# Kernel tuning notes

Measured on AMD Instinct MI355X. Metric: run time of the kernel, lower is better.

The kernel has to match this reference:

```python
import jax, jax.numpy as jnp
import numpy as np

D_MODEL, D_STATE, D_CONV, EXPAND = 1024, 16, 4, 2
D_INNER = EXPAND * D_MODEL
BATCH, SEQ = 2, 2048


def setup_inputs() -> dict:
    key = jax.random.key(0)
    ks = jax.random.split(key, 10)
    s = lambda fan_in: 1.0 / np.sqrt(fan_in)
    return {
        "x": jax.random.normal(ks[0], (BATCH, SEQ, D_MODEL), jnp.float32),
        "W_in": jax.random.normal(ks[1], (2 * D_INNER, D_MODEL), jnp.float32) * s(D_MODEL),
        "w_conv": jax.random.normal(ks[2], (D_INNER, D_CONV), jnp.float32) * s(D_CONV),
        "b_conv": jax.random.normal(ks[3], (D_INNER,), jnp.float32) * 0.02,
        "W_x": jax.random.normal(ks[4], (D_INNER + 2 * D_STATE, D_INNER), jnp.float32) * s(D_INNER),
        "W_dt": jax.random.normal(ks[5], (D_INNER, D_INNER), jnp.float32) * s(D_INNER),
        "b_dt": jax.random.normal(ks[6], (D_INNER,), jnp.float32) * 0.02,
        "A_log": jnp.log(jax.random.uniform(ks[7], (D_INNER, D_STATE), jnp.float32, 1e-4, 1.0)),
        "D": jnp.ones((D_INNER,), jnp.float32),
        "W_out": jax.random.normal(ks[8], (D_MODEL, D_INNER), jnp.float32) * s(D_INNER),
    }


def _depthwise_causal_conv(x, w, b):
    # x: (B, L, C), w: (C, K), causal (left-pad K-1), matches conv1d(padding=K-1)[..., :L]
    K = w.shape[1]
    L = x.shape[1]
    xp = jnp.pad(x, ((0, 0), (K - 1, 0), (0, 0)))
    out = b
    for k in range(K):  # K is tiny (4)
        out = out + xp[:, k:k + L, :] * w[:, k]
    return out


def _selective_scan(x, delta, Bm, Cm, A, Dv):
    # x, delta: (B, L, d_inner); Bm, Cm: (B, L, d_state)
    def step(state, inp):
        x_t, d_t, B_t, C_t = inp  # (B,d_inner),(B,d_inner),(B,d_state),(B,d_state)
        decay = jnp.exp(d_t[..., None] * A)          # (B, d_inner, d_state)
        state = decay * state + B_t[:, None, :] * x_t[..., None]
        y_t = jnp.einsum('bds,bs->bd', state, C_t) + x_t * Dv
        return state, y_t

    init = jnp.zeros((x.shape[0], x.shape[2], A.shape[1]), x.dtype)
    xs = tuple(jnp.swapaxes(a, 0, 1) for a in (x, delta, Bm, Cm))
    _, ys = jax.lax.scan(step, init, xs)             # ys: (L, B, d_inner)
    return jnp.swapaxes(ys, 0, 1)


def reference(x, W_in, w_conv, b_conv, W_x, W_dt, b_dt, A_log, D, W_out):
    silu = jax.nn.silu
    xz = x @ W_in.T                                   # (B, L, 2*d_inner)
    x_inner, z = jnp.split(xz, 2, axis=-1)
    x_conv = silu(_depthwise_causal_conv(x_inner, w_conv, b_conv))
    x_dbl = x_conv @ W_x.T                            # (B, L, d_inner + 2*d_state)
    delta, Bm, Cm = jnp.split(x_dbl, [D_INNER, D_INNER + D_STATE], axis=-1)
    delta = jax.nn.softplus(delta @ W_dt.T + b_dt)
    A = -jnp.exp(A_log.astype(jnp.float32))
    y = _selective_scan(x_conv, delta, Bm, Cm, A, D)
    y = y * silu(z)
    return y @ W_out.T
```

## Files before the change

kernel.cpp:

```cpp
#include <hip/hip_runtime.h>
#include <hip/hip_bf16.h>


#define BATCH 2
#define SEQ   2048
#define DM    1024
#define DI    2048
#define DS    16
#define T_TOK (BATCH * SEQ)

#define CL 64
#define NC 32

typedef __bf16 v8bf __attribute__((ext_vector_type(8)));
typedef float  v4f  __attribute__((ext_vector_type(4)));

__device__ __forceinline__ void gld16(const void* g, void* l) {
    __builtin_amdgcn_global_load_lds(
        (const __attribute__((address_space(1))) void*)g,
        (__attribute__((address_space(3))) void*)l, 16, 0, 0);
}

__device__ __forceinline__ float b2f(__hip_bfloat16 v) { return __bfloat162float(v); }

__global__ void detect_dtype(const unsigned* __restrict__ Dptr, int* __restrict__ flag) {
    if (threadIdx.x == 0 && blockIdx.x == 0)
        *flag = (Dptr[0] == 0x3F803F80u) ? 1 : 0;
}

__device__ __forceinline__ float load_in(const void* p, size_t i, int isbf) {
    return isbf ? b2f(((const __hip_bfloat16*)p)[i]) : ((const float*)p)[i];
}

#define NBIG0 (T_TOK * DM)
#define NBIG1 (4096 * DM)
#define NBIG2 (DI * DI)
#define NBIG3 (DM * DI)
__global__ void convert_big(const void* __restrict__ s0, const void* __restrict__ s1,
                            const void* __restrict__ s2, const void* __restrict__ s3,
                            __hip_bfloat16* __restrict__ d0, __hip_bfloat16* __restrict__ d1,
                            __hip_bfloat16* __restrict__ d2, __hip_bfloat16* __restrict__ d3,
                            const int* __restrict__ flag) {
    if (*flag) return;
    size_t e = ((size_t)blockIdx.x * 256 + threadIdx.x) * 8;
    const float* src; __hip_bfloat16* dst;
    if (e < NBIG0)                      { src = (const float*)s0 + e;                 dst = d0 + e; }
    else if (e < NBIG0 + NBIG1)         { e -= NBIG0; src = (const float*)s1 + e;     dst = d1 + e; }
    else if (e < NBIG0 + NBIG1 + NBIG2) { e -= NBIG0 + NBIG1; src = (const float*)s2 + e; dst = d2 + e; }
    else                                { e -= NBIG0 + NBIG1 + NBIG2; src = (const float*)s3 + e; dst = d3 + e; }
    const float4 a = *(const float4*)src;
    const float4 b = *(const float4*)(src + 4);
    __bf16 o[8] = {(__bf16)a.x,(__bf16)a.y,(__bf16)a.z,(__bf16)a.w,
                   (__bf16)b.x,(__bf16)b.y,(__bf16)b.z,(__bf16)b.w};
    *(uint4*)dst = *(uint4*)&o[0];
}

__global__ void convert_small(const void* __restrict__ wconv, const void* __restrict__ bconv,
                              const void* __restrict__ bdt, const void* __restrict__ dv,
                              __hip_bfloat16* __restrict__ wconvb, __hip_bfloat16* __restrict__ bconvb,
                              __hip_bfloat16* __restrict__ bdtb, __hip_bfloat16* __restrict__ db,
                              const int* __restrict__ flag) {
    const int isbf = *flag;
    const int i = blockIdx.x * 256 + threadIdx.x;
    if (i < 8192)        wconvb[i]        = __float2bfloat16(load_in(wconv, i, isbf));
    else if (i < 10240)  bconvb[i - 8192] = __float2bfloat16(load_in(bconv, i - 8192, isbf));
    else if (i < 12288)  bdtb[i - 10240]  = __float2bfloat16(load_in(bdt, i - 10240, isbf));
    else if (i < 14336)  db[i - 12288]    = __float2bfloat16(load_in(dv, i - 12288, isbf));
}

template <int MODE, int KDIM>
__global__ __launch_bounds__(512, 2) void gemm8p(
    const __hip_bfloat16* __restrict__ Ac, const void* __restrict__ Araw,
    const __hip_bfloat16* __restrict__ Bc, const void* __restrict__ Braw,
    void* __restrict__ out0, void* __restrict__ out1,
    const __hip_bfloat16* __restrict__ bias,
    const int* __restrict__ flag,
    int N)
{
    constexpr int NT = KDIM >> 5;
    __shared__ v8bf lds[8192];

    const int isbf = *flag;
    const __hip_bfloat16* A  = (isbf && Araw) ? (const __hip_bfloat16*)Araw : Ac;
    const __hip_bfloat16* Bw = (isbf && Braw) ? (const __hip_bfloat16*)Braw : Bc;

    const int nx = gridDim.x;
    const int nblk = nx * gridDim.y;
    const int id = blockIdx.y * nx + blockIdx.x;
    const int sid = (id & 7) * (nblk >> 3) + (id >> 3);
    const int bm = (sid / nx) * 256;
    const int bn = (sid % nx) * 256;

    const int tid   = threadIdx.x;
    const int lane  = tid & 63;
    const int w     = tid >> 6;
    const int wr    = (w >> 2) * 128;
    const int wc    = (w & 3) * 64;
    const int lrow  = lane & 15;
    const int lquad = lane >> 4;
    const int swz   = lquad ^ ((lrow >> 1) & 3);

    v4f acc[8][4];
#pragma unroll
    for (int i = 0; i < 8; i++)
#pragma unroll
        for (int j = 0; j < 4; j++) acc[i][j] = (v4f){0.f, 0.f, 0.f, 0.f};

    const int r0 = tid >> 2;
    const int q0 = (tid & 3) ^ ((r0 >> 1) & 3);
    const __hip_bfloat16* gA0 = A  + (size_t)(bm + r0) * KDIM + q0 * 8;
    const __hip_bfloat16* gA1 = gA0 + (size_t)128 * KDIM;
    const __hip_bfloat16* gB0 = Bw + (size_t)(bn + r0) * KDIM + q0 * 8;
    const __hip_bfloat16* gB1 = gB0 + (size_t)128 * KDIM;
    char* lbase = (char*)&lds[0] + tid * 16;

    int sA[8], sB[4];
#pragma unroll
    for (int i = 0; i < 8; i++) sA[i] = (wr + i * 16 + lrow) * 4 + swz;
#pragma unroll
    for (int i = 0; i < 4; i++) sB[i] = 1024 + (wc + i * 16 + lrow) * 4 + swz;

#define STAGE8(kt, b) do {                         \
        const size_t ko_ = (size_t)(kt) * 32;      \
        char* d_ = lbase + (b) * 32768;            \
        gld16(gA0 + ko_, d_);                      \
        gld16(gA1 + ko_, d_ + 8192);               \
        gld16(gB0 + ko_, d_ + 16384);              \
        gld16(gB1 + ko_, d_ + 24576);              \
    } while (0)

    STAGE8(0, 0);
    STAGE8(1, 1);
    STAGE8(2, 2);

#pragma unroll 4
    for (int t = 0; t < NT; ++t) {
        const int cb = t & 3;
        if (t + 3 < NT) {
            STAGE8(t + 3, (t + 3) & 3);
            asm volatile("s_waitcnt vmcnt(12)" ::: "memory");
        } else if (t + 3 == NT) {
            asm volatile("s_waitcnt vmcnt(8)" ::: "memory");
        } else if (t + 2 == NT) {
            asm volatile("s_waitcnt vmcnt(4)" ::: "memory");
        } else {
            asm volatile("s_waitcnt vmcnt(0)" ::: "memory");
        }
        __builtin_amdgcn_s_barrier();

        const v8bf* buf = &lds[0] + cb * 2048;
        v8bf af[8], bfr[4];
#pragma unroll
        for (int i = 0; i < 8; i++) af[i] = buf[sA[i]];
#pragma unroll
        for (int i = 0; i < 4; i++) bfr[i] = buf[sB[i]];
        asm volatile("s_waitcnt lgkmcnt(0)" ::: "memory");
        __builtin_amdgcn_s_barrier();

        __builtin_amdgcn_s_setprio(1);
#pragma unroll
        for (int mi = 0; mi < 8; mi++)
#pragma unroll
            for (int ni = 0; ni < 4; ni++)
                acc[mi][ni] = __builtin_amdgcn_mfma_f32_16x16x32_bf16(
                    af[mi], bfr[ni], acc[mi][ni], 0, 0, 0);
        __builtin_amdgcn_s_setprio(0);
    }
#undef STAGE8

#pragma unroll
    for (int mi = 0; mi < 8; mi++) {
#pragma unroll
        for (int ni = 0; ni < 4; ni++) {
#pragma unroll
            for (int r = 0; r < 4; r++) {
                const int grow = bm + wr + mi * 16 + lquad * 4 + r;
                const int gcol = bn + wc + ni * 16 + lrow;
                const float v = acc[mi][ni][r];
                if (MODE == 0) {
                    ((__hip_bfloat16*)out0)[(size_t)grow * N + gcol] = __float2bfloat16(v);
                } else if (MODE == 1) {
                    if (gcol < 2048) {
                        ((__hip_bfloat16*)out0)[(size_t)grow * 2048 + gcol] = __float2bfloat16(v);
                    } else if (gcol < 2080) {
                        ((float*)out1)[(size_t)grow * 32 + (gcol - 2048)] = v;
                    }
                } else {
                    const float x = v + b2f(bias[gcol]);
                    const float sp = (x > 15.f) ? x : __logf(1.f + __expf(x));
                    ((__hip_bfloat16*)out0)[(size_t)grow * 2048 + gcol] = __float2bfloat16(sp);
                }
            }
        }
    }
}

template <int MODE, int TN>
__global__ __launch_bounds__(256) void gemm_bt(
    const __hip_bfloat16* __restrict__ Ac, const void* __restrict__ Araw,
    const __hip_bfloat16* __restrict__ Bc, const void* __restrict__ Braw,
    void* __restrict__ out0, void* __restrict__ out1,
    const __hip_bfloat16* __restrict__ bias,
    const int* __restrict__ flag,
    int M, int N, int K)
{
    constexpr int NF = TN / 32;
    constexpr int ASLOT = 512;
    constexpr int BSLOT = TN * 4;
    __shared__ v8bf Asv[2 * ASLOT];
    __shared__ v8bf Bsv[2 * BSLOT];

    const int isbf = *flag;
    const __hip_bfloat16* A  = (isbf && Araw) ? (const __hip_bfloat16*)Araw : Ac;
    const __hip_bfloat16* Bw = (isbf && Braw) ? (const __hip_bfloat16*)Braw : Bc;

    const int nx = gridDim.x;
    const int nblk = nx * gridDim.y;
    const int id = blockIdx.y * nx + blockIdx.x;
    const int sid = (id & 7) * (nblk >> 3) + (id >> 3);
    const int bxs = sid % nx;
    const int bys = sid / nx;

    const int tid  = threadIdx.x;
    const int bm   = bys * 128;
    const int bn   = bxs * TN;
    const int w    = tid >> 6;
    const int lane = tid & 63;
    const int wm   = (w >> 1) * 64;
    const int wn   = (w & 1) * (TN / 2);
    const int lrow  = lane & 15;
    const int lquad = lane >> 4;

    v4f acc[4][NF];
#pragma unroll
    for (int i = 0; i < 4; i++)
#pragma unroll
        for (int j = 0; j < NF; j++) acc[i][j] = (v4f){0.f, 0.f, 0.f, 0.f};

    const int r0 = tid >> 2;
    const int q0 = (tid & 3) ^ ((r0 >> 1) & 3);
    const __hip_bfloat16* gA0 = A  + (size_t)(bm + r0) * K + q0 * 8;
    const __hip_bfloat16* gA1 = A  + (size_t)(bm + 64 + r0) * K + q0 * 8;
    const __hip_bfloat16* gB0 = Bw + (size_t)(bn + r0) * K + q0 * 8;
    const __hip_bfloat16* gB1 = Bw + (size_t)(bn + 64 + r0) * K + q0 * 8;
    char* lA0 = (char*)Asv + tid * 16;
    char* lA1 = (char*)Asv + 4096 + tid * 16;
    char* lB0 = (char*)Bsv + tid * 16;
    char* lB1 = (char*)Bsv + 4096 + tid * 16;

    const int swz = lquad ^ ((lrow >> 1) & 3);
    int sA[4], sB[NF];
#pragma unroll
    for (int i = 0; i < 4; i++) sA[i] = (wm + i * 16 + lrow) * 4 + swz;
#pragma unroll
    for (int i = 0; i < NF; i++) sB[i] = (wn + i * 16 + lrow) * 4 + swz;

    const int NIT = K >> 5;
    gld16(gA0, lA0);
    gld16(gA1, lA1);
    gld16(gB0, lB0);
    if (TN == 128) gld16(gB1, lB1);

    int k = 32;
    for (int it = 0; it < NIT; ++it) {
        const int cb = it & 1;
        __syncthreads();
        if (it + 1 < NIT) {
            const int pa = (cb ^ 1) * 8192;
            const int pb = (cb ^ 1) * (BSLOT * 16);
            gld16(gA0 + k, lA0 + pa);
            gld16(gA1 + k, lA1 + pa);
            gld16(gB0 + k, lB0 + pb);
            if (TN == 128) gld16(gB1 + k, lB1 + pb);
            k += 32;
        }
        const int ca = cb * ASLOT;
        const int cbb = cb * BSLOT;
        v8bf af[4], bfr[NF];
#pragma unroll
        for (int i = 0; i < 4; i++)
            af[i] = Asv[ca + sA[i]];
#pragma unroll
        for (int i = 0; i < NF; i++)
            bfr[i] = Bsv[cbb + sB[i]];
#pragma unroll
        for (int mi = 0; mi < 4; mi++)
#pragma unroll
            for (int ni = 0; ni < NF; ni++)
                acc[mi][ni] = __builtin_amdgcn_mfma_f32_16x16x32_bf16(
                    af[mi], bfr[ni], acc[mi][ni], 0, 0, 0);
    }

#pragma unroll
    for (int mi = 0; mi < 4; mi++) {
#pragma unroll
        for (int ni = 0; ni < NF; ni++) {
#pragma unroll
            for (int r = 0; r < 4; r++) {
                const int grow = bm + wm + mi * 16 + lquad * 4 + r;
                const int gcol = bn + wn + ni * 16 + lrow;
                const float v = acc[mi][ni][r];
                if (MODE == 0) {
                    ((__hip_bfloat16*)out0)[(size_t)grow * N + gcol] = __float2bfloat16(v);
                } else if (MODE == 1) {
                    if (gcol < 2048) {
                        ((__hip_bfloat16*)out0)[(size_t)grow * 2048 + gcol] = __float2bfloat16(v);
                    } else if (gcol < 2080) {
                        ((float*)out1)[(size_t)grow * 32 + (gcol - 2048)] = v;
                    }
                } else if (MODE == 2) {
                    const float x = v + b2f(bias[gcol]);
                    const float sp = (x > 15.f) ? x : __logf(1.f + __expf(x));
                    ((__hip_bfloat16*)out0)[(size_t)grow * 2048 + gcol] = __float2bfloat16(sp);
                } else {
                    if (isbf)
                        ((__hip_bfloat16*)out0)[(size_t)grow * N + gcol] = __float2bfloat16(v);
                    else
                        ((float*)out0)[(size_t)grow * N + gcol] = v;
                }
            }
        }
    }
}

__global__ void prep_A(const void* __restrict__ A_log, float* __restrict__ Amat,
                       const int* __restrict__ flag) {
    const int isbf = *flag;
    const int i = blockIdx.x * 256 + threadIdx.x;
    if (i < DI * DS) Amat[i] = -__expf(load_in(A_log, i, isbf));
}

__global__ void pad_Wx(const void* __restrict__ Wx, __hip_bfloat16* __restrict__ Wxp,
                       const int* __restrict__ flag) {
    const int isbf = *flag;
    const size_t e = ((size_t)blockIdx.x * 256 + threadIdx.x) * 8;
    if (e >= (size_t)2304 * 2048) return;
    if (e >= (size_t)2080 * 2048) {
        __bf16 z[8] = {};
        *(uint4*)(Wxp + e) = *(uint4*)&z[0];
        return;
    }
    if (isbf) {
        *(uint4*)(Wxp + e) = *(const uint4*)((const __hip_bfloat16*)Wx + e);
    } else {
        const float* src = (const float*)Wx + e;
        const float4 a = *(const float4*)src;
        const float4 b = *(const float4*)(src + 4);
        __bf16 o[8] = {(__bf16)a.x,(__bf16)a.y,(__bf16)a.z,(__bf16)a.w,
                       (__bf16)b.x,(__bf16)b.y,(__bf16)b.z,(__bf16)b.w};
        *(uint4*)(Wxp + e) = *(uint4*)&o[0];
    }
}

__global__ __launch_bounds__(256) void conv_silu(
    const __hip_bfloat16* __restrict__ xz,
    const __hip_bfloat16* __restrict__ wconv,
    const __hip_bfloat16* __restrict__ bconv,
    __hip_bfloat16* __restrict__ xconv)
{
    const int idx = blockIdx.x * 256 + threadIdx.x;
    const int c8 = (idx & 255) << 3;
    const int tg = idx >> 8;
    const int tl = tg & (SEQ - 1);

    __bf16 wl[32], bl[8];
    *(uint4*)&wl[0]  = *(const uint4*)(wconv + c8 * 4);
    *(uint4*)&wl[8]  = *(const uint4*)(wconv + c8 * 4 + 8);
    *(uint4*)&wl[16] = *(const uint4*)(wconv + c8 * 4 + 16);
    *(uint4*)&wl[24] = *(const uint4*)(wconv + c8 * 4 + 24);
    *(uint4*)&bl[0]  = *(const uint4*)(bconv + c8);

    float acc[8];
#pragma unroll
    for (int cc = 0; cc < 8; cc++) acc[cc] = (float)bl[cc];

#pragma unroll
    for (int k = 0; k < 4; k++) {
        const int ts = tl - 3 + k;
        if (ts >= 0) {
            __bf16 xl[8];
            *(uint4*)&xl[0] = *(const uint4*)(xz + (size_t)(tg - 3 + k) * 4096 + c8);
#pragma unroll
            for (int cc = 0; cc < 8; cc++)
                acc[cc] += (float)wl[cc * 4 + k] * (float)xl[cc];
        }
    }

    __bf16 o[8];
#pragma unroll
    for (int cc = 0; cc < 8; cc++) {
        const float s = acc[cc] / (1.f + __expf(-acc[cc]));
        o[cc] = (__bf16)s;
    }
    *(uint4*)(xconv + (size_t)tg * DI + c8) = *(uint4*)&o[0];
}

__global__ __launch_bounds__(256) void scan_p1(
    const __hip_bfloat16* __restrict__ delta, const __hip_bfloat16* __restrict__ xconv,
    const float* __restrict__ BC, const float* __restrict__ Amat,
    float* __restrict__ Pws, float* __restrict__ Sws)
{
    const int d = blockIdx.x * 256 + threadIdx.x;
    const int c = blockIdx.y;
    const int b = blockIdx.z;
    const int tg0 = b * SEQ + c * CL;

    __shared__ float bc[CL * 32];
    for (int i = threadIdx.x; i < CL * 32; i += 256) bc[i] = BC[(size_t)tg0 * 32 + i];
    __syncthreads();

    float Areg[DS];
#pragma unroll
    for (int s = 0; s < DS; s++) Areg[s] = Amat[d * DS + s];

    float P[DS], S[DS];
#pragma unroll
    for (int s = 0; s < DS; s++) { P[s] = 1.f; S[s] = 0.f; }

    for (int i = 0; i < CL; i++) {
        const size_t tg = tg0 + i;
        const float dl = b2f(delta[tg * DI + d]);
        const float x  = b2f(xconv[tg * DI + d]);
#pragma unroll
        for (int s = 0; s < DS; s++) {
            const float e = __expf(dl * Areg[s]);
            P[s] *= e;
            S[s] = e * S[s] + bc[i * 32 + s] * x;
        }
    }

    const size_t base = (((size_t)b * NC + c) * DI + d) * DS;
#pragma unroll
    for (int s = 0; s < DS; s += 4) {
        *(float4*)(Pws + base + s) = make_float4(P[s], P[s+1], P[s+2], P[s+3]);
        *(float4*)(Sws + base + s) = make_float4(S[s], S[s+1], S[s+2], S[s+3]);
    }
}

__global__ void scan_p2(float* __restrict__ Pws, float* __restrict__ Sws) {
    const int idx = blockIdx.x * 256 + threadIdx.x;
    const int b  = idx >> 15;
    const int ds = idx & 32767;
    float carry = 0.f;
    for (int c = 0; c < NC; c++) {
        const size_t a = (((size_t)b * NC + c) << 15) + ds;
        const float p  = Pws[a];
        const float sv = Sws[a];
        Sws[a] = carry;
        carry = p * carry + sv;
    }
}

__global__ __launch_bounds__(256) void scan_p3(
    const __hip_bfloat16* __restrict__ delta, const __hip_bfloat16* __restrict__ xconv,
    const float* __restrict__ BC, const float* __restrict__ Amat,
    const float* __restrict__ Sws, const __hip_bfloat16* __restrict__ xz,
    const __hip_bfloat16* __restrict__ Dv, __hip_bfloat16* __restrict__ yg)
{
    const int d = blockIdx.x * 256 + threadIdx.x;
    const int c = blockIdx.y;
    const int b = blockIdx.z;
    const int tg0 = b * SEQ + c * CL;

    __shared__ float bc[CL * 32];
    for (int i = threadIdx.x; i < CL * 32; i += 256) bc[i] = BC[(size_t)tg0 * 32 + i];
    __syncthreads();

    float Areg[DS];
#pragma unroll
    for (int s = 0; s < DS; s++) Areg[s] = Amat[d * DS + s];

    const size_t base = (((size_t)b * NC + c) * DI + d) * DS;
    float S[DS];
#pragma unroll
    for (int s = 0; s < DS; s += 4) {
        const float4 v = *(const float4*)(Sws + base + s);
        S[s] = v.x; S[s+1] = v.y; S[s+2] = v.z; S[s+3] = v.w;
    }
    const float Dd = b2f(Dv[d]);

    for (int i = 0; i < CL; i++) {
        const size_t tg = tg0 + i;
        const float dl = b2f(delta[tg * DI + d]);
        const float x  = b2f(xconv[tg * DI + d]);
        float y = 0.f;
#pragma unroll
        for (int s = 0; s < DS; s++) {
            const float e = __expf(dl * Areg[s]);
            S[s] = e * S[s] + bc[i * 32 + s] * x;
            y += S[s] * bc[i * 32 + 16 + s];
        }
        y += x * Dd;
        const float z = b2f(xz[tg * 4096 + 2048 + d]);
        const float g = z / (1.f + __expf(-z));
        yg[tg * DI + d] = __float2bfloat16(y * g);
    }
}

extern "C" void kernel_launch(void* const* d_in, const int* in_sizes, int n_in,
                              void* d_out, int out_size, void* d_ws, size_t ws_size,
                              hipStream_t stream)
{
    const void* x_raw     = d_in[0];
    const void* W_in_raw  = d_in[1];
    const void* wconv_raw = d_in[2];
    const void* bconv_raw = d_in[3];
    const void* W_x_raw   = d_in[4];
    const void* W_dt_raw  = d_in[5];
    const void* b_dt_raw  = d_in[6];
    const void* A_log_raw = d_in[7];
    const void* D_raw     = d_in[8];
    const void* W_out_raw = d_in[9];

    char* ws = (char*)d_ws;
    size_t off = 0;
    auto alloc = [&](size_t bytes) { char* p = ws + off; off += (bytes + 255) & ~(size_t)255; return p; };
    int*            FLAG  = (int*)alloc(256);
    __hip_bfloat16* XB    = (__hip_bfloat16*)alloc((size_t)T_TOK * DM * 2);
    __hip_bfloat16* WINB  = (__hip_bfloat16*)alloc((size_t)4096 * DM * 2);
    __hip_bfloat16* WDTB  = (__hip_bfloat16*)alloc((size_t)DI * DI * 2);
    __hip_bfloat16* WOUTB = (__hip_bfloat16*)alloc((size_t)DM * DI * 2);
    __hip_bfloat16* WCONVB= (__hip_bfloat16*)alloc((size_t)DI * 4 * 2);
    __hip_bfloat16* BCONVB= (__hip_bfloat16*)alloc((size_t)DI * 2);
    __hip_bfloat16* BDTB  = (__hip_bfloat16*)alloc((size_t)DI * 2);
    __hip_bfloat16* DB    = (__hip_bfloat16*)alloc((size_t)DI * 2);
    __hip_bfloat16* XZ    = (__hip_bfloat16*)alloc((size_t)T_TOK * 4096 * 2);
    __hip_bfloat16* XCONV = (__hip_bfloat16*)alloc((size_t)T_TOK * DI * 2);
    __hip_bfloat16* DRAW  = (__hip_bfloat16*)alloc((size_t)T_TOK * DI * 2);
    __hip_bfloat16* WXPAD = (__hip_bfloat16*)alloc((size_t)2304 * DI * 2);
    float*          BC    = (float*)alloc((size_t)T_TOK * 32 * 4);
    __hip_bfloat16* DELTA = (__hip_bfloat16*)alloc((size_t)T_TOK * DI * 2);
    float*          AMAT  = (float*)alloc((size_t)DI * DS * 4);
    float*          PWS   = (float*)alloc((size_t)BATCH * NC * DI * DS * 4);
    float*          SWS   = (float*)alloc((size_t)BATCH * NC * DI * DS * 4);
    __hip_bfloat16* YG    = (__hip_bfloat16*)alloc((size_t)T_TOK * DI * 2);

    detect_dtype<<<1, 64, 0, stream>>>((const unsigned*)D_raw, FLAG);
    convert_big<<<(NBIG0 + NBIG1 + NBIG2 + NBIG3) / (256 * 8), 256, 0, stream>>>(
        x_raw, W_in_raw, W_dt_raw, W_out_raw, XB, WINB, WDTB, WOUTB, FLAG);
    convert_small<<<56, 256, 0, stream>>>(wconv_raw, bconv_raw, b_dt_raw, D_raw,
                                          WCONVB, BCONVB, BDTB, DB, FLAG);
    prep_A<<<(DI * DS + 255) / 256, 256, 0, stream>>>(A_log_raw, AMAT, FLAG);
    pad_Wx<<<(int)(((size_t)2304 * 2048 / 8 + 255) / 256), 256, 0, stream>>>(W_x_raw, WXPAD, FLAG);

    gemm8p<0, 1024><<<dim3(16, 16), 512, 0, stream>>>(
        XB, x_raw, WINB, W_in_raw, XZ, nullptr, nullptr, FLAG, 4096);

    conv_silu<<<T_TOK, 256, 0, stream>>>(XZ, WCONVB, BCONVB, XCONV);

    gemm8p<1, 2048><<<dim3(9, 16), 512, 0, stream>>>(
        XCONV, nullptr, WXPAD, nullptr, DRAW, BC, nullptr, FLAG, 2304);

    gemm8p<2, 2048><<<dim3(8, 16), 512, 0, stream>>>(
        DRAW, nullptr, WDTB, W_dt_raw, DELTA, nullptr, BDTB, FLAG, 2048);

    scan_p1<<<dim3(DI / 256, NC, BATCH), 256, 0, stream>>>(DELTA, XCONV, BC, AMAT, PWS, SWS);
    scan_p2<<<(BATCH * DI * DS) / 256, 256, 0, stream>>>(PWS, SWS);
    scan_p3<<<dim3(DI / 256, NC, BATCH), 256, 0, stream>>>(DELTA, XCONV, BC, AMAT, SWS, XZ, DB, YG);

    gemm_bt<3, 64><<<dim3(16, 32), 256, 0, stream>>>(
        YG, nullptr, WOUTB, W_out_raw, d_out, nullptr, nullptr, FLAG, T_TOK, DM, DI);
}
```

Baseline: 468.7 us.

## Split GEMM k-step into two half-phases interleaving LDS reads, prefetch and MFMA

Restructures the GEMM main loop into two phases per k-tile. Each phase issues half the global-to-LDS prefetch and half the A-fragment LDS reads, then runs 16 MFMAs, with barriers and the vmcnt waits rebalanced between phases. The aim is to overlap LDS reads and global loads with matrix-core work instead of loading everything before computing. It adds more barriers per iteration, and the hand-tuned vmcnt accounting must stay correct for the tail iterations.

```diff
diff --git a/kernel.cpp b/kernel.cpp
--- a/kernel.cpp
+++ b/kernel.cpp
@@ -132,39 +132,62 @@
     STAGE8(0, 0);
     STAGE8(1, 1);
     STAGE8(2, 2);
+    asm volatile("s_waitcnt vmcnt(8)" ::: "memory");
+    __builtin_amdgcn_s_barrier();
 
 #pragma unroll 4
     for (int t = 0; t < NT; ++t) {
         const int cb = t & 3;
-        if (t + 3 < NT) {
-            STAGE8(t + 3, (t + 3) & 3);
-            asm volatile("s_waitcnt vmcnt(12)" ::: "memory");
-        } else if (t + 3 == NT) {
-            asm volatile("s_waitcnt vmcnt(8)" ::: "memory");
-        } else if (t + 2 == NT) {
-            asm volatile("s_waitcnt vmcnt(4)" ::: "memory");
-        } else {
-            asm volatile("s_waitcnt vmcnt(0)" ::: "memory");
+        const v8bf* buf = &lds[0] + cb * 2048;
+        const int pf = t + 3;
+        char* pdst = lbase + (pf & 3) * 32768;
+        const size_t pko = (size_t)pf * 32;
+
+        v8bf af0[4], af1[4], bfr[4];
+#pragma unroll
+        for (int i = 0; i < 4; i++) af0[i] = buf[sA[i]];
+#pragma unroll
+        for (int i = 0; i < 4; i++) bfr[i] = buf[sB[i]];
+        if (pf < NT) {
+            gld16(gA0 + pko, pdst);
+            gld16(gA1 + pko, pdst + 8192);
         }
         __builtin_amdgcn_s_barrier();
-
-        const v8bf* buf = &lds[0] + cb * 2048;
-        v8bf af[8], bfr[4];
-#pragma unroll
-        for (int i = 0; i < 8; i++) af[i] = buf[sA[i]];
-#pragma unroll
-        for (int i = 0; i < 4; i++) bfr[i] = buf[sB[i]];
         asm volatile("s_waitcnt lgkmcnt(0)" ::: "memory");
-        __builtin_amdgcn_s_barrier();
-
+        __builtin_amdgcn_sched_barrier(0);
         __builtin_amdgcn_s_setprio(1);
 #pragma unroll
-        for (int mi = 0; mi < 8; mi++)
+        for (int mi = 0; mi < 4; mi++)
 #pragma unroll
             for (int ni = 0; ni < 4; ni++)
                 acc[mi][ni] = __builtin_amdgcn_mfma_f32_16x16x32_bf16(
-                    af[mi], bfr[ni], acc[mi][ni], 0, 0, 0);
+                    af0[mi], bfr[ni], acc[mi][ni], 0, 0, 0);
         __builtin_amdgcn_s_setprio(0);
+        __builtin_amdgcn_s_barrier();
+
+#pragma unroll
+        for (int i = 0; i < 4; i++) af1[i] = buf[sA[4 + i]];
+        if (pf < NT) {
+            gld16(gB0 + pko, pdst + 16384);
+            gld16(gB1 + pko, pdst + 24576);
+            asm volatile("s_waitcnt vmcnt(8)" ::: "memory");
+        } else if (t + 3 == NT) {
+            asm volatile("s_waitcnt vmcnt(4)" ::: "memory");
+        } else if (t + 2 == NT) {
+            asm volatile("s_waitcnt vmcnt(0)" ::: "memory");
+        }
+        __builtin_amdgcn_s_barrier();
+        asm volatile("s_waitcnt lgkmcnt(0)" ::: "memory");
+        __builtin_amdgcn_sched_barrier(0);
+        __builtin_amdgcn_s_setprio(1);
+#pragma unroll
+        for (int mi = 0; mi < 4; mi++)
+#pragma unroll
+            for (int ni = 0; ni < 4; ni++)
+                acc[4 + mi][ni] = __builtin_amdgcn_mfma_f32_16x16x32_bf16(
+                    af1[mi], bfr[ni], acc[4 + mi][ni], 0, 0, 0);
+        __builtin_amdgcn_s_setprio(0);
+        __builtin_amdgcn_s_barrier();
     }
 #undef STAGE8
 
```

Result: no change. 465.3 us (-0.7%).
